# Kernel optimization log

Hardware: AMD Instinct MI355X
Metric: run time of the kernel (lower is better)

The kernel has to match this reference:

```python
import jax, jax.numpy as jnp
import numpy as np
import math

EMBED_DIM = 1024
NUM_HEADS = 16
HEAD_DIM = EMBED_DIM // NUM_HEADS
B, S = 2, 2048


def setup_inputs() -> dict:
    key = jax.random.key(0)
    ks = jax.random.split(key, 5)
    scale = 1.0 / math.sqrt(EMBED_DIM)
    x = jax.random.normal(ks[0], (B, S, EMBED_DIM), dtype=jnp.float32)
    W_q = jax.random.normal(ks[1], (EMBED_DIM, EMBED_DIM), dtype=jnp.float32) * scale
    W_k = jax.random.normal(ks[2], (EMBED_DIM, EMBED_DIM), dtype=jnp.float32) * scale
    W_v = jax.random.normal(ks[3], (EMBED_DIM, EMBED_DIM), dtype=jnp.float32) * scale
    W_o = jax.random.normal(ks[4], (EMBED_DIM, EMBED_DIM), dtype=jnp.float32) * scale
    # causal mask: True = masked out (matches torch masked_fill semantics)
    mask = jnp.triu(jnp.ones((S, S), dtype=bool), k=1)
    return {"x": x, "mask": mask, "W_q": W_q, "W_k": W_k, "W_v": W_v, "W_o": W_o}


def _split_heads(x):
    b, s, _ = x.shape
    return x.reshape(b, s, NUM_HEADS, HEAD_DIM).transpose(0, 2, 1, 3)  # [b,h,s,hd]


def reference(x, mask, W_q, W_k, W_v, W_o):
    # torch nn.Linear(bias=False): y = x @ W.T
    Q = _split_heads(x @ W_q.T)
    K = _split_heads(x @ W_k.T)
    V = _split_heads(x @ W_v.T)
    scale = 1.0 / math.sqrt(HEAD_DIM)
    scores = jnp.einsum("bhqd,bhkd->bhqk", Q, K) * scale  # [b,h,s,s]
    scores = jnp.where(mask[None, None, :, :], -jnp.inf, scores)
    weights = jax.nn.softmax(scores, axis=-1)
    out = jnp.einsum("bhqk,bhkd->bhqd", weights, V)
    out = out.transpose(0, 2, 1, 3).reshape(x.shape[0], x.shape[1], EMBED_DIM)
    return out @ W_o.T
```

## Files before the change

kernel.cpp:

```cpp
#include <hip/hip_runtime.h>
#include <hip/hip_bf16.h>

typedef short bf16x8 __attribute__((ext_vector_type(8)));
typedef unsigned short u16x8 __attribute__((ext_vector_type(8)));
typedef unsigned short u16x4 __attribute__((ext_vector_type(4)));
typedef float f32x4 __attribute__((ext_vector_type(4)));

typedef unsigned int __attribute__((address_space(1))) gu32;
typedef unsigned int __attribute__((address_space(3))) lu32;

#define MFMA16(a, b, c) __builtin_amdgcn_mfma_f32_16x16x32_bf16((a), (b), (c), 0, 0, 0)

constexpr int SEQ = 2048;
constexpr int NH = 16;
constexpr int NTOK = 2 * SEQ;

__device__ __forceinline__ float bf2f(unsigned short u) {
  union { unsigned int i; float f; } v; v.i = ((unsigned int)u) << 16; return v.f;
}
__device__ __forceinline__ unsigned short f2bf(float f) {
  __hip_bfloat16 h = __float2bfloat16(f);
  return __builtin_bit_cast(unsigned short, h);
}
__device__ __forceinline__ unsigned int pkbf_trunc(float hi, float lo) {
  return __builtin_amdgcn_perm(__builtin_bit_cast(unsigned int, hi),
                               __builtin_bit_cast(unsigned int, lo), 0x07060302u);
}
__device__ __forceinline__ u16x8 cvt8(const float* __restrict__ p) {
  f32x4 a = *(const f32x4*)p;
  f32x4 b = *(const f32x4*)(p + 4);
  u16x8 r;
#pragma unroll
  for (int j = 0; j < 4; j++) { r[j] = f2bf(a[j]); r[4 + j] = f2bf(b[j]); }
  return r;
}

__global__ __launch_bounds__(256) void cvt_all(
    const float* __restrict__ x, const float* __restrict__ wq, const float* __restrict__ wk,
    const float* __restrict__ wv, const float* __restrict__ wo,
    unsigned short* __restrict__ Xb, unsigned short* __restrict__ Wb) {
  const int z = blockIdx.y;
  const float* src = (z == 0) ? x : (z == 1) ? wq : (z == 2) ? wk : (z == 3) ? wv : wo;
  unsigned short* dst = (z == 0) ? Xb : Wb + (size_t)(z - 1) * 1024 * 1024;
  const int n = (z == 0) ? NTOK * 1024 : 1024 * 1024;
  for (int i = (blockIdx.x * 256 + threadIdx.x) * 8; i < n; i += gridDim.x * 256 * 8)
    *(u16x8*)(dst + i) = cvt8(src + i);
}

template <int ROWS, int NWAVE>
__device__ __forceinline__ void stage_glds(const unsigned short* __restrict__ gbase,
                                           int rstride,
                                           unsigned short* __restrict__ lds,
                                           int wid, int lane) {
  constexpr int ISS = ROWS * 8 / (NWAVE * 64);
#pragma unroll
  for (int t = 0; t < ISS; ++t) {
    const int slot = (wid * ISS + t) * 64 + lane;
    const int row = slot >> 3;
    const int c8 = (slot & 7) ^ (row & 7);
    const unsigned short* gp = gbase + (size_t)row * rstride + c8 * 8;
    unsigned short* lp = lds + (size_t)(wid * ISS + t) * 512;
    __builtin_amdgcn_global_load_lds((const gu32*)gp, (lu32*)lp, 16, 0, 0);
  }
}

__device__ __forceinline__ bf16x8 frag_ld(const unsigned short* __restrict__ lds, int row, int c8) {
  const int slot = row * 8 + (c8 ^ (row & 7));
  return *(const bf16x8*)(lds + slot * 8);
}

template <int BM, int BN, int LDC, bool CF32>
__global__ __launch_bounds__(256) void gemm_lds(
    const unsigned short* __restrict__ A,
    const unsigned short* __restrict__ B,
    void* __restrict__ Cv) {
  constexpr int K = 1024;
  constexpr int MI = BM / 32, NI = BN / 32;

  __shared__ __align__(16) unsigned short As[BM * 64];
  __shared__ __align__(16) unsigned short Bs[BN * 64];

  const int tid = threadIdx.x;
  const int wid = tid >> 6;
  const int lane = tid & 63;
  const int quad = lane >> 4;
  const int c16 = lane & 15;
  const int wrow = wid >> 1, wcol = wid & 1;

  const int m0 = blockIdx.x * BM;
  const int n0 = blockIdx.y * BN;

  f32x4 acc[MI][NI];
#pragma unroll
  for (int i = 0; i < MI; i++)
#pragma unroll
    for (int j = 0; j < NI; j++) acc[i][j] = f32x4{0.f, 0.f, 0.f, 0.f};

  for (int kb = 0; kb < K; kb += 64) {
    __syncthreads();
    stage_glds<BM, 4>(A + (size_t)m0 * K + kb, K, As, wid, lane);
    stage_glds<BN, 4>(B + (size_t)n0 * K + kb, K, Bs, wid, lane);
    __syncthreads();
#pragma unroll
    for (int ks = 0; ks < 2; ++ks) {
      bf16x8 af[MI], bfr[NI];
#pragma unroll
      for (int i = 0; i < MI; i++)
        af[i] = frag_ld(As, wrow * (BM / 2) + i * 16 + c16, ks * 4 + quad);
#pragma unroll
      for (int j = 0; j < NI; j++)
        bfr[j] = frag_ld(Bs, wcol * (BN / 2) + j * 16 + c16, ks * 4 + quad);
#pragma unroll
      for (int i = 0; i < MI; i++)
#pragma unroll
        for (int j = 0; j < NI; j++) acc[i][j] = MFMA16(af[i], bfr[j], acc[i][j]);
    }
  }

#pragma unroll
  for (int i = 0; i < MI; i++) {
#pragma unroll
    for (int j = 0; j < NI; j++) {
      int row = m0 + wrow * (BM / 2) + i * 16 + quad * 4;
      int col = n0 + wcol * (BN / 2) + j * 16 + c16;
#pragma unroll
      for (int r = 0; r < 4; r++) {
        if constexpr (CF32) ((float*)Cv)[(size_t)(row + r) * LDC + col] = acc[i][j][r];
        else ((unsigned short*)Cv)[(size_t)(row + r) * LDC + col] = f2bf(acc[i][j][r]);
      }
    }
  }
}

#define SBAR do { __builtin_amdgcn_sched_barrier(0); \
                  asm volatile("s_barrier" ::: "memory"); \
                  __builtin_amdgcn_sched_barrier(0); } while (0)

__global__ __launch_bounds__(512) void gemm_8ph_w192(
    const unsigned short* __restrict__ A,
    const unsigned short* __restrict__ B,
    unsigned short* __restrict__ C) {
  constexpr int K = 1024;
  __shared__ __align__(16) unsigned short As[2][256 * 64];
  __shared__ __align__(16) unsigned short Bs[2][192 * 64];

  const int tid = threadIdx.x;
  const int wid = tid >> 6, lane = tid & 63;
  const int quad = lane >> 4, c16 = lane & 15;
  const int wr = wid >> 2;
  const int wc = wid & 3;

  const int bid = blockIdx.x;
  const int swz = (bid & 7) * 32 + (bid >> 3);
  const int m0 = (swz >> 4) * 256;
  const int n0 = (swz & 15) * 192;

  const unsigned short* Abase = A + (size_t)m0 * K;
  const unsigned short* Bbase = B + (size_t)n0 * K;

  f32x4 acc[8][3];
#pragma unroll
  for (int i = 0; i < 8; i++)
#pragma unroll
    for (int j = 0; j < 3; j++) acc[i][j] = f32x4{0.f, 0.f, 0.f, 0.f};

  bf16x8 af[4];
  bf16x8 bf0[3];
  bf16x8 bf1[3];

  auto lda4 = [&](const unsigned short* asb, int mo, int ks) {
#pragma unroll
    for (int mi = 0; mi < 4; mi++)
      af[mi] = frag_ld(asb, wr * 128 + (mo + mi) * 16 + c16, ks * 4 + quad);
  };
  auto ldb3 = [&](const unsigned short* bsb, bf16x8 (&bf)[3], int ks) {
#pragma unroll
    for (int ni = 0; ni < 3; ni++)
      bf[ni] = frag_ld(bsb, wc * 48 + ni * 16 + c16, ks * 4 + quad);
  };
  auto mm12 = [&](bf16x8 (&bf)[3], int mo) {
    __builtin_amdgcn_s_setprio(1);
#pragma unroll
    for (int mi = 0; mi < 4; mi++)
#pragma unroll
      for (int ni = 0; ni < 3; ni++)
        acc[mo + mi][ni] = MFMA16(af[mi], bf[ni], acc[mo + mi][ni]);
    __builtin_amdgcn_s_setprio(0);
  };

  stage_glds<192, 8>(Bbase, K, Bs[0], wid, lane);
  stage_glds<128, 8>(Abase, K, As[0], wid, lane);
  stage_glds<128, 8>(Abase + (size_t)128 * K, K, As[0] + 8192, wid, lane);
  stage_glds<192, 8>(Bbase + 64, K, Bs[1], wid, lane);
  asm volatile("s_waitcnt vmcnt(3)" ::: "memory");
  SBAR;

  for (int i = 0; i < 7; ++i) {
    const int t = 2 * i;
    const int kb1 = (t + 1) * 64, kb2 = (t + 2) * 64, kb3 = (t + 3) * 64;
    lda4(As[0], 0, 0); ldb3(Bs[0], bf0, 0);
    stage_glds<128, 8>(Abase + kb1, K, As[1], wid, lane);
    mm12(bf0, 0); SBAR;
    lda4(As[0], 0, 1); ldb3(Bs[0], bf1, 1);
    stage_glds<128, 8>(Abase + (size_t)128 * K + kb1, K, As[1] + 8192, wid, lane);
    mm12(bf1, 0); SBAR;
    lda4(As[0], 4, 0);
    stage_glds<192, 8>(Bbase + kb2, K, Bs[0], wid, lane);
    mm12(bf0, 4); SBAR;
    lda4(As[0], 4, 1);
    asm volatile("s_waitcnt vmcnt(3)" ::: "memory");
    mm12(bf1, 4); SBAR;
    lda4(As[1], 0, 0); ldb3(Bs[1], bf0, 0);
    stage_glds<128, 8>(Abase + kb2, K, As[0], wid, lane);
    mm12(bf0, 0); SBAR;
    lda4(As[1], 0, 1); ldb3(Bs[1], bf1, 1);
    stage_glds<128, 8>(Abase + (size_t)128 * K + kb2, K, As[0] + 8192, wid, lane);
    mm12(bf1, 0); SBAR;
    lda4(As[1], 4, 0);
    stage_glds<192, 8>(Bbase + kb3, K, Bs[1], wid, lane);
    mm12(bf0, 4); SBAR;
    lda4(As[1], 4, 1);
    asm volatile("s_waitcnt vmcnt(3)" ::: "memory");
    mm12(bf1, 4); SBAR;
  }

  {
    const int kb1 = 15 * 64;
    lda4(As[0], 0, 0); ldb3(Bs[0], bf0, 0);
    stage_glds<128, 8>(Abase + kb1, K, As[1], wid, lane);
    mm12(bf0, 0); SBAR;
    lda4(As[0], 0, 1); ldb3(Bs[0], bf1, 1);
    stage_glds<128, 8>(Abase + (size_t)128 * K + kb1, K, As[1] + 8192, wid, lane);
    mm12(bf1, 0); SBAR;
    lda4(As[0], 4, 0);
    mm12(bf0, 4); SBAR;
    lda4(As[0], 4, 1);
    asm volatile("s_waitcnt vmcnt(0)" ::: "memory");
    mm12(bf1, 4); SBAR;
    lda4(As[1], 0, 0); ldb3(Bs[1], bf0, 0);
    mm12(bf0, 0); SBAR;
    lda4(As[1], 0, 1); ldb3(Bs[1], bf1, 1);
    mm12(bf1, 0); SBAR;
    lda4(As[1], 4, 0);
    mm12(bf0, 4); SBAR;
    lda4(As[1], 4, 1);
    mm12(bf1, 4);
  }

#pragma unroll
  for (int mi = 0; mi < 8; mi++) {
#pragma unroll
    for (int ni = 0; ni < 3; ni++) {
      const int row = m0 + wr * 128 + mi * 16 + quad * 4;
      const int col = n0 + wc * 48 + ni * 16 + c16;
#pragma unroll
      for (int r = 0; r < 4; r++)
        C[(size_t)(row + r) * 3072 + col] = f2bf(acc[mi][ni][r]);
    }
  }
}

__device__ __forceinline__ int vt_idx(int d, int kv) {
  int ck = kv >> 3;
  int s = ((d >> 3) ^ d) & 7;
  return d * 64 + ((ck ^ s) << 3) + (kv & 7);
}

struct AttnShared {
  unsigned short Kt[2][64 * 64];
  unsigned short Vt[2][64 * 64];
  unsigned short Pt[4][16 * 64];
};

__global__ __launch_bounds__(256) void attn_kernel(
    const unsigned short* __restrict__ QKV,
    unsigned short* __restrict__ Oa) {
  __shared__ AttnShared sh;
  const int h = blockIdx.x;
  const int b = blockIdx.y;
  const int t = 31 - blockIdx.z;
  const int tid = threadIdx.x;
  const int wid = tid >> 6, lane = tid & 63;
  const int quad = lane >> 4, c16 = lane & 15;
  const size_t tokbase = (size_t)b * SEQ;
  const int q0 = t * 64;
  const int nkv = t + 1;

  const unsigned short* qp = QKV + (tokbase + q0 + wid * 16 + c16) * 3072 + h * 64;
  bf16x8 qf[2];
#pragma unroll
  for (int ks = 0; ks < 2; ++ks) {
    u16x8 u = *(const u16x8*)(qp + ks * 32 + quad * 8);
    bf16x8 tq;
#pragma unroll
    for (int j = 0; j < 8; j++) tq[j] = (short)f2bf(0.1803368801f * bf2f(u[j]));
    qf[ks] = tq;
  }

  const unsigned short* kbase = QKV + tokbase * 3072 + 1024 + h * 64;
  const unsigned short* vbase = QKV + tokbase * 3072 + 2048 + h * 64;
  const int vkv = (tid >> 4) * 4;
  const int vd = (tid & 15) * 4;

  f32x4 o[4];
  float lacc = 0.f;
#pragma unroll
  for (int nt = 0; nt < 4; nt++) o[nt] = f32x4{0.f, 0.f, 0.f, 0.f};
  unsigned short* PtW = sh.Pt[wid];
  const int pt_sub = (quad & 1) * 4;
  const int pt_c8h = quad >> 1;

  stage_glds<64, 4>(kbase, 3072, sh.Kt[0], wid, lane);
  u16x4 vr[4];
#pragma unroll
  for (int i = 0; i < 4; i++)
    vr[i] = *(const u16x4*)(vbase + (size_t)(vkv + i) * 3072 + vd);
#pragma unroll
  for (int dd = 0; dd < 4; ++dd) {
    uint2 w;
    w.x = (unsigned int)vr[0][dd] | ((unsigned int)vr[1][dd] << 16);
    w.y = (unsigned int)vr[2][dd] | ((unsigned int)vr[3][dd] << 16);
    *(uint2*)&sh.Vt[0][vt_idx(vd + dd, vkv)] = w;
  }

  for (int kt = 0; kt < nkv; ++kt) {
    const int buf = kt & 1;
    __syncthreads();

    const bool pf = (kt + 1 < nkv);
    if (pf) {
      const size_t nofs = (size_t)(kt + 1) * 64;
      stage_glds<64, 4>(kbase + nofs * 3072, 3072, sh.Kt[buf ^ 1], wid, lane);
#pragma unroll
      for (int i = 0; i < 4; i++)
        vr[i] = *(const u16x4*)(vbase + (nofs + vkv + i) * 3072 + vd);
    }

    const unsigned short* KtB = sh.Kt[buf];
    f32x4 st[4];
    __builtin_amdgcn_s_setprio(1);
#pragma unroll
    for (int nt = 0; nt < 4; ++nt) {
      f32x4 a = f32x4{-16.f, -16.f, -16.f, -16.f};
      a = MFMA16(frag_ld(KtB, nt * 16 + c16, quad), qf[0], a);
      a = MFMA16(frag_ld(KtB, nt * 16 + c16, 4 + quad), qf[1], a);
      st[nt] = a;
    }
    __builtin_amdgcn_s_setprio(0);
    if (kt == nkv - 1) {
      const int kv0 = kt * 64;
      const int qg = q0 + wid * 16 + c16;
#pragma unroll
      for (int nt = 0; nt < 4; nt++)
#pragma unroll
        for (int r = 0; r < 4; r++) {
          int kg = kv0 + nt * 16 + quad * 4 + r;
          if (kg > qg) st[nt][r] = -1e30f;
        }
    }

#pragma unroll
    for (int nt = 0; nt < 4; nt++) {
      float p0 = __builtin_amdgcn_exp2f(st[nt][0]);
      float p1 = __builtin_amdgcn_exp2f(st[nt][1]);
      float p2 = __builtin_amdgcn_exp2f(st[nt][2]);
      float p3 = __builtin_amdgcn_exp2f(st[nt][3]);
      lacc += (p0 + p1) + (p2 + p3);
      uint2 w;
      w.x = pkbf_trunc(p1, p0);
      w.y = pkbf_trunc(p3, p2);
      const int c8w = 2 * nt + pt_c8h;
      const int slot = c16 * 8 + (c8w ^ (c16 & 7));
      *(uint2*)&PtW[slot * 8 + pt_sub] = w;
    }

    if (pf) {
#pragma unroll
      for (int dd = 0; dd < 4; ++dd) {
        uint2 w;
        w.x = (unsigned int)vr[0][dd] | ((unsigned int)vr[1][dd] << 16);
        w.y = (unsigned int)vr[2][dd] | ((unsigned int)vr[3][dd] << 16);
        *(uint2*)&sh.Vt[buf ^ 1][vt_idx(vd + dd, vkv)] = w;
      }
    }

    const unsigned short* VtB = sh.Vt[buf];
    __builtin_amdgcn_s_setprio(1);
#pragma unroll
    for (int ks = 0; ks < 2; ++ks) {
      bf16x8 pfrag = frag_ld(PtW, c16, ks * 4 + quad);
#pragma unroll
      for (int nt2 = 0; nt2 < 4; ++nt2) {
        bf16x8 vf = *(const bf16x8*)&VtB[vt_idx(nt2 * 16 + c16, ks * 32 + quad * 8)];
        o[nt2] = MFMA16(vf, pfrag, o[nt2]);
      }
    }
    __builtin_amdgcn_s_setprio(0);
  }

  lacc += __shfl_xor(lacc, 16);
  lacc += __shfl_xor(lacc, 32);
  const float linv = 1.f / lacc;
  const size_t row = tokbase + q0 + wid * 16 + c16;
#pragma unroll
  for (int nt2 = 0; nt2 < 4; nt2++) {
    uint2 w;
    w.x = (unsigned int)f2bf(o[nt2][0] * linv) | ((unsigned int)f2bf(o[nt2][1] * linv) << 16);
    w.y = (unsigned int)f2bf(o[nt2][2] * linv) | ((unsigned int)f2bf(o[nt2][3] * linv) << 16);
    *(uint2*)&Oa[row * 1024 + h * 64 + nt2 * 16 + quad * 4] = w;
  }
}

template <int BM, int BN, int LDC, bool AF32, bool CF32>
__global__ __launch_bounds__(256) void gemm_bt(
    const void* __restrict__ Av, const float* __restrict__ W0, const float* __restrict__ W1,
    const float* __restrict__ W2, void* __restrict__ Cv) {
  constexpr int K = 1024;
  constexpr int LDS_LD = 72;
  constexpr int MI = BM / 32, NI = BN / 32;
  __shared__ __align__(16) unsigned short As[BM][LDS_LD];
  __shared__ __align__(16) unsigned short Bs[BN][LDS_LD];
  const int tid = threadIdx.x, wid = tid >> 6, lane = tid & 63;
  const int quad = lane >> 4, c16 = lane & 15;
  const int wrow = wid >> 1, wcol = wid & 1;
  const float* W = (blockIdx.z == 0) ? W0 : (blockIdx.z == 1 ? W1 : W2);
  const int m0 = blockIdx.y * BM, n0 = blockIdx.x * BN, cofs = blockIdx.z * 1024;
  f32x4 acc[MI][NI];
#pragma unroll
  for (int i = 0; i < MI; i++)
#pragma unroll
    for (int j = 0; j < NI; j++) acc[i][j] = f32x4{0.f, 0.f, 0.f, 0.f};
  for (int kb = 0; kb < K; kb += 64) {
    __syncthreads();
#pragma unroll
    for (int c = tid; c < BM * 8; c += 256) {
      int row = c >> 3, c8 = c & 7;
      if constexpr (AF32)
        *(u16x8*)&As[row][c8 * 8] = cvt8((const float*)Av + (size_t)(m0 + row) * K + kb + c8 * 8);
      else
        *(u16x8*)&As[row][c8 * 8] = *(const u16x8*)((const unsigned short*)Av + (size_t)(m0 + row) * K + kb + c8 * 8);
    }
#pragma unroll
    for (int c = tid; c < BN * 8; c += 256) {
      int row = c >> 3, c8 = c & 7;
      *(u16x8*)&Bs[row][c8 * 8] = cvt8(W + (size_t)(n0 + row) * K + kb + c8 * 8);
    }
    __syncthreads();
#pragma unroll
    for (int ks = 0; ks < 2; ++ks) {
      bf16x8 af[MI], bfr[NI];
#pragma unroll
      for (int i = 0; i < MI; i++)
        af[i] = *(const bf16x8*)&As[wrow * (BM / 2) + i * 16 + c16][ks * 32 + quad * 8];
#pragma unroll
      for (int j = 0; j < NI; j++)
        bfr[j] = *(const bf16x8*)&Bs[wcol * (BN / 2) + j * 16 + c16][ks * 32 + quad * 8];
#pragma unroll
      for (int i = 0; i < MI; i++)
#pragma unroll
        for (int j = 0; j < NI; j++) acc[i][j] = MFMA16(af[i], bfr[j], acc[i][j]);
    }
  }
#pragma unroll
  for (int i = 0; i < MI; i++)
#pragma unroll
    for (int j = 0; j < NI; j++) {
      int row = m0 + wrow * (BM / 2) + i * 16 + quad * 4;
      int col = n0 + wcol * (BN / 2) + j * 16 + c16 + cofs;
#pragma unroll
      for (int r = 0; r < 4; r++) {
        if constexpr (CF32) ((float*)Cv)[(size_t)(row + r) * LDC + col] = acc[i][j][r];
        else ((unsigned short*)Cv)[(size_t)(row + r) * LDC + col] = f2bf(acc[i][j][r]);
      }
    }
}

extern "C" void kernel_launch(void* const* d_in, const int* in_sizes, int n_in,
                              void* d_out, int out_size, void* d_ws, size_t ws_size,
                              hipStream_t stream) {
  const float* x = (const float*)d_in[0];
  const float* Wq = (const float*)d_in[2];
  const float* Wk = (const float*)d_in[3];
  const float* Wv = (const float*)d_in[4];
  const float* Wo = (const float*)d_in[5];
  float* out = (float*)d_out;

  unsigned short* QKV = (unsigned short*)d_ws;
  unsigned short* Wb = QKV + (size_t)NTOK * 3072;
  unsigned short* Xb = Wb + (size_t)4 * 1024 * 1024;
  unsigned short* AT = Xb;

  if (ws_size >= (size_t)40 * 1024 * 1024) {
    cvt_all<<<dim3(256, 5), 256, 0, stream>>>(x, Wq, Wk, Wv, Wo, Xb, Wb);
    gemm_8ph_w192<<<dim3(256), 512, 0, stream>>>(Xb, Wb, QKV);
    attn_kernel<<<dim3(NH, 2, 32), 256, 0, stream>>>(QKV, AT);
    gemm_lds<128, 64, 1024, true><<<dim3(32, 16), 256, 0, stream>>>(
        AT, Wb + (size_t)3 * 1024 * 1024, out);
  } else {
    unsigned short* QKV2 = (unsigned short*)d_ws;
    unsigned short* AT2 = QKV2 + (size_t)NTOK * 3072;
    gemm_bt<128, 128, 3072, true, false><<<dim3(8, 32, 3), 256, 0, stream>>>(x, Wq, Wk, Wv, QKV2);
    attn_kernel<<<dim3(NH, 2, 32), 256, 0, stream>>>(QKV2, AT2);
    gemm_bt<64, 64, 1024, false, true><<<dim3(16, 64, 1), 256, 0, stream>>>(AT2, Wo, Wo, Wo, out);
  }
}
```

Measured before the change: 172.8 us.

## Replace output projection GEMM with double-buffered pipelined kernel

Swaps the simple single-buffered output-projection GEMM for a new kernel with double-buffered LDS. Each next K-tile's global-to-LDS loads are issued while MFMAs run on the current tile, using split A/B staging, partial vmcnt waits and raw s_barrier. It also adds MFMA priority boosting and a block-index swizzle for better L2 locality. The aim is to hide global load latency and cut the two syncthreads per K step, in exchange for twice the LDS and more fragile hand-scheduled waitcnt logic.

```diff
diff --git a/kernel.cpp b/kernel.cpp
--- a/kernel.cpp
+++ b/kernel.cpp
@@ -67,69 +67,6 @@
 __device__ __forceinline__ bf16x8 frag_ld(const unsigned short* __restrict__ lds, int row, int c8) {
   const int slot = row * 8 + (c8 ^ (row & 7));
   return *(const bf16x8*)(lds + slot * 8);
-}
-
-template <int BM, int BN, int LDC, bool CF32>
-__global__ __launch_bounds__(256) void gemm_lds(
-    const unsigned short* __restrict__ A,
-    const unsigned short* __restrict__ B,
-    void* __restrict__ Cv) {
-  constexpr int K = 1024;
-  constexpr int MI = BM / 32, NI = BN / 32;
-
-  __shared__ __align__(16) unsigned short As[BM * 64];
-  __shared__ __align__(16) unsigned short Bs[BN * 64];
-
-  const int tid = threadIdx.x;
-  const int wid = tid >> 6;
-  const int lane = tid & 63;
-  const int quad = lane >> 4;
-  const int c16 = lane & 15;
-  const int wrow = wid >> 1, wcol = wid & 1;
-
-  const int m0 = blockIdx.x * BM;
-  const int n0 = blockIdx.y * BN;
-
-  f32x4 acc[MI][NI];
-#pragma unroll
-  for (int i = 0; i < MI; i++)
-#pragma unroll
-    for (int j = 0; j < NI; j++) acc[i][j] = f32x4{0.f, 0.f, 0.f, 0.f};
-
-  for (int kb = 0; kb < K; kb += 64) {
-    __syncthreads();
-    stage_glds<BM, 4>(A + (size_t)m0 * K + kb, K, As, wid, lane);
-    stage_glds<BN, 4>(B + (size_t)n0 * K + kb, K, Bs, wid, lane);
-    __syncthreads();
-#pragma unroll
-    for (int ks = 0; ks < 2; ++ks) {
-      bf16x8 af[MI], bfr[NI];
-#pragma unroll
-      for (int i = 0; i < MI; i++)
-        af[i] = frag_ld(As, wrow * (BM / 2) + i * 16 + c16, ks * 4 + quad);
-#pragma unroll
-      for (int j = 0; j < NI; j++)
-        bfr[j] = frag_ld(Bs, wcol * (BN / 2) + j * 16 + c16, ks * 4 + quad);
-#pragma unroll
-      for (int i = 0; i < MI; i++)
-#pragma unroll
-        for (int j = 0; j < NI; j++) acc[i][j] = MFMA16(af[i], bfr[j], acc[i][j]);
-    }
-  }
-
-#pragma unroll
-  for (int i = 0; i < MI; i++) {
-#pragma unroll
-    for (int j = 0; j < NI; j++) {
-      int row = m0 + wrow * (BM / 2) + i * 16 + quad * 4;
-      int col = n0 + wcol * (BN / 2) + j * 16 + c16;
-#pragma unroll
-      for (int r = 0; r < 4; r++) {
-        if constexpr (CF32) ((float*)Cv)[(size_t)(row + r) * LDC + col] = acc[i][j][r];
-        else ((unsigned short*)Cv)[(size_t)(row + r) * LDC + col] = f2bf(acc[i][j][r]);
-      }
-    }
-  }
 }
 
 #define SBAR do { __builtin_amdgcn_sched_barrier(0); \
@@ -260,6 +197,114 @@
   }
 }
 
+__global__ __launch_bounds__(256) void gemm_op_2ph(
+    const unsigned short* __restrict__ A,
+    const unsigned short* __restrict__ B,
+    float* __restrict__ C) {
+  constexpr int K = 1024;
+  __shared__ __align__(16) unsigned short As[2][128 * 64];
+  __shared__ __align__(16) unsigned short Bs[2][64 * 64];
+
+  const int tid = threadIdx.x;
+  const int wid = tid >> 6, lane = tid & 63;
+  const int quad = lane >> 4, c16 = lane & 15;
+  const int wr = wid >> 1, wc = wid & 1;
+
+  const int bid = blockIdx.x;
+  const int swz = (bid & 7) * 64 + (bid >> 3);
+  const int m0 = (swz >> 4) * 128;
+  const int n0 = (swz & 15) * 64;
+
+  const unsigned short* Abase = A + (size_t)m0 * K;
+  const unsigned short* Bbase = B + (size_t)n0 * K;
+
+  f32x4 acc[4][2];
+#pragma unroll
+  for (int i = 0; i < 4; i++)
+#pragma unroll
+    for (int j = 0; j < 2; j++) acc[i][j] = f32x4{0.f, 0.f, 0.f, 0.f};
+
+  bf16x8 af[2][2];
+  bf16x8 bf[2][2];
+
+  auto lda22 = [&](const unsigned short* asb, int mo) {
+#pragma unroll
+    for (int mi = 0; mi < 2; mi++)
+#pragma unroll
+      for (int ks = 0; ks < 2; ks++)
+        af[mi][ks] = frag_ld(asb, wr * 64 + (mo + mi) * 16 + c16, ks * 4 + quad);
+  };
+  auto ldb22 = [&](const unsigned short* bsb) {
+#pragma unroll
+    for (int ni = 0; ni < 2; ni++)
+#pragma unroll
+      for (int ks = 0; ks < 2; ks++)
+        bf[ni][ks] = frag_ld(bsb, wc * 32 + ni * 16 + c16, ks * 4 + quad);
+  };
+  auto mm8 = [&](int mo) {
+    __builtin_amdgcn_s_setprio(1);
+#pragma unroll
+    for (int mi = 0; mi < 2; mi++)
+#pragma unroll
+      for (int ni = 0; ni < 2; ni++)
+#pragma unroll
+        for (int ks = 0; ks < 2; ks++)
+          acc[mo + mi][ni] = MFMA16(af[mi][ks], bf[ni][ks], acc[mo + mi][ni]);
+    __builtin_amdgcn_s_setprio(0);
+  };
+
+  stage_glds<64, 4>(Bbase, K, Bs[0], wid, lane);
+  stage_glds<128, 4>(Abase, K, As[0], wid, lane);
+  stage_glds<64, 4>(Bbase + 64, K, Bs[1], wid, lane);
+  asm volatile("s_waitcnt vmcnt(2)" ::: "memory");
+  SBAR;
+
+  for (int i = 0; i < 7; ++i) {
+    const int t = 2 * i;
+    const int kb1 = (t + 1) * 64, kb2 = (t + 2) * 64, kb3 = (t + 3) * 64;
+    lda22(As[0], 0); ldb22(Bs[0]);
+    stage_glds<128, 4>(Abase + kb1, K, As[1], wid, lane);
+    mm8(0); SBAR;
+    lda22(As[0], 2);
+    stage_glds<64, 4>(Bbase + kb2, K, Bs[0], wid, lane);
+    asm volatile("s_waitcnt vmcnt(2)" ::: "memory");
+    mm8(2); SBAR;
+    lda22(As[1], 0); ldb22(Bs[1]);
+    stage_glds<128, 4>(Abase + kb2, K, As[0], wid, lane);
+    mm8(0); SBAR;
+    lda22(As[1], 2);
+    stage_glds<64, 4>(Bbase + kb3, K, Bs[1], wid, lane);
+    asm volatile("s_waitcnt vmcnt(2)" ::: "memory");
+    mm8(2); SBAR;
+  }
+
+  {
+    const int kb1 = 15 * 64;
+    lda22(As[0], 0); ldb22(Bs[0]);
+    stage_glds<128, 4>(Abase + kb1, K, As[1], wid, lane);
+    mm8(0); SBAR;
+    lda22(As[0], 2);
+    asm volatile("s_waitcnt vmcnt(0)" ::: "memory");
+    mm8(2); SBAR;
+    lda22(As[1], 0); ldb22(Bs[1]);
+    mm8(0); SBAR;
+    lda22(As[1], 2);
+    mm8(2);
+  }
+
+#pragma unroll
+  for (int a = 0; a < 4; a++) {
+#pragma unroll
+    for (int ni = 0; ni < 2; ni++) {
+      const int row = m0 + wr * 64 + a * 16 + quad * 4;
+      const int col = n0 + wc * 32 + ni * 16 + c16;
+#pragma unroll
+      for (int r = 0; r < 4; r++)
+        C[(size_t)(row + r) * 1024 + col] = acc[a][ni][r];
+    }
+  }
+}
+
 __device__ __forceinline__ int vt_idx(int d, int kv) {
   int ck = kv >> 3;
   int s = ((d >> 3) ^ d) & 7;
@@ -494,7 +539,7 @@
     cvt_all<<<dim3(256, 5), 256, 0, stream>>>(x, Wq, Wk, Wv, Wo, Xb, Wb);
     gemm_8ph_w192<<<dim3(256), 512, 0, stream>>>(Xb, Wb, QKV);
     attn_kernel<<<dim3(NH, 2, 32), 256, 0, stream>>>(QKV, AT);
-    gemm_lds<128, 64, 1024, true><<<dim3(32, 16), 256, 0, stream>>>(
+    gemm_op_2ph<<<dim3(512), 256, 0, stream>>>(
         AT, Wb + (size_t)3 * 1024 * 1024, out);
   } else {
     unsigned short* QKV2 = (unsigned short*)d_ws;
```

After: 174.2 us. Within noise of the previous version (+0.8%).
